# Kernel tuning notes

Hardware: AMD Instinct MI355X
Metric: run time of the kernel (lower is better)

## Reference

```python
import jax, jax.numpy as jnp
import numpy as np

DIM = 2048
K_DIM = 2048
Q_HEADS = 16
KV_HEADS = 4
HEAD_DIM = DIM // Q_HEADS  # 128
KV_DIM = HEAD_DIM * KV_HEADS  # 512
MAX_LEN = 2048
ROPE_THETA = 10000.0
ROPE_FACTOR = 8.0


def _rope_cos_sin(seq_len):
    # Faithful to generate_sin_cos_pos_emb with is_causal=True
    d = HEAD_DIM
    seq_eff = max(seq_len, MAX_LEN)
    base_adj = (ROPE_FACTOR * seq_eff / MAX_LEN - (ROPE_FACTOR - 1.0)) ** (d / (d - 2))
    adjusted_base = ROPE_THETA * base_adj
    inv_freq = 1.0 / adjusted_base ** (np.arange(0, d, 2, dtype=np.float32) / d)
    pos = np.arange(seq_len, dtype=np.float32)  # causal: no centering
    freqs = pos[:, None] * inv_freq[None, :]            # [S, d/2]
    emb = np.concatenate([freqs, freqs], axis=-1)        # [S, d]
    return jnp.asarray(np.cos(emb), jnp.float32), jnp.asarray(np.sin(emb), jnp.float32)


def _rotate_half(x):
    x1, x2 = jnp.split(x, 2, axis=-1)
    return jnp.concatenate([-x2, x1], axis=-1)


def setup_inputs() -> dict:
    key = jax.random.key(0)
    ks = jax.random.split(key, 12)
    B, S = 1, 2048
    s_in = 1.0 / np.sqrt(DIM)
    s_k = 1.0 / np.sqrt(K_DIM)
    return {
        "query": jax.random.normal(ks[0], (B, S, DIM), jnp.float32),
        "key": jax.random.normal(ks[1], (B, S, K_DIM), jnp.float32),
        "value": jax.random.normal(ks[2], (B, S, K_DIM), jnp.float32),
        "Wq": jax.random.uniform(ks[3], (DIM, DIM), jnp.float32, -s_in, s_in),
        "bq": jax.random.uniform(ks[4], (DIM,), jnp.float32, -s_in, s_in),
        "Wk": jax.random.uniform(ks[5], (KV_DIM, K_DIM), jnp.float32, -s_k, s_k),
        "bk": jax.random.uniform(ks[6], (KV_DIM,), jnp.float32, -s_k, s_k),
        "Wv": jax.random.uniform(ks[7], (KV_DIM, K_DIM), jnp.float32, -s_k, s_k),
        "bv": jax.random.uniform(ks[8], (KV_DIM,), jnp.float32, -s_k, s_k),
        "Wo": jax.random.uniform(ks[9], (DIM, DIM), jnp.float32, -s_in, s_in),
        "bo": jax.random.uniform(ks[10], (DIM,), jnp.float32, -s_in, s_in),
    }


def reference(query, key, value, Wq, bq, Wk, bk, Wv, bv, Wo, bo):
    B, S, _ = query.shape
    scale = HEAD_DIM ** -0.5

    q = query @ Wq.T + bq                                   # [B,S,DIM]
    k = key @ Wk.T + bk                                     # [B,S,KV_DIM]
    v = value @ Wv.T + bv                                   # [B,S,KV_DIM]

    q = q.reshape(B, S, Q_HEADS, HEAD_DIM)
    k = k.reshape(B, S, KV_HEADS, HEAD_DIM)
    v = v.reshape(B, S, KV_HEADS, HEAD_DIM)

    cos, sin = _rope_cos_sin(S)                              # [S,D]
    cos = cos[None, :, None, :]
    sin = sin[None, :, None, :]
    q = q * cos + _rotate_half(q) * sin
    k = k * cos + _rotate_half(k) * sin

    # [B,H,S,D]
    q = q.transpose(0, 2, 1, 3)
    k = k.transpose(0, 2, 1, 3)
    v = v.transpose(0, 2, 1, 3)

    rep = Q_HEADS // KV_HEADS
    k = jnp.repeat(k, rep, axis=1)
    v = jnp.repeat(v, rep, axis=1)

    scores = jnp.einsum('bhqd,bhkd->bhqk', q, k) * scale
    causal = jnp.tril(jnp.ones((S, S), bool))
    scores = jnp.where(causal[None, None], scores, jnp.finfo(scores.dtype).min)
    attn = jax.nn.softmax(scores, axis=-1)
    out = jnp.einsum('bhqk,bhkd->bhqd', attn, v)             # [B,H,S,D]

    out = out.transpose(0, 2, 1, 3).reshape(B, S, DIM)
    return out @ Wo.T + bo
```

## Files before the change

kernel.cpp:

```cpp
#include <hip/hip_runtime.h>
#include <stdint.h>

typedef __attribute__((ext_vector_type(8))) short short8;
typedef __attribute__((ext_vector_type(4))) float f32x4;
typedef __attribute__((ext_vector_type(4))) unsigned short u16x4;
typedef unsigned short bf16_t;

__device__ __forceinline__ bf16_t f2bf(float f) {
  union { float f; uint32_t u; } x; x.f = f;
  uint32_t r = x.u + 0x7fffu + ((x.u >> 16) & 1u);
  return (bf16_t)(r >> 16);
}

__device__ __forceinline__ void ld_g2l_16(const bf16_t* g, bf16_t* l) {
  __builtin_amdgcn_global_load_lds(
      (const __attribute__((address_space(1))) void*)g,
      (__attribute__((address_space(3))) void*)l, 16, 0, 0);
}

__global__ void rope_tab(float* __restrict__ CS, float* __restrict__ SN) {
  int idx = blockIdx.x * 256 + threadIdx.x;
  int i = idx & 63, pos = idx >> 6;
  float ang = (float)pos * exp2f((float)i * -0.2076205059f);
  CS[idx] = cosf(ang);
  SN[idx] = sinf(ang);
}

__global__ void convert_all(const float* __restrict__ s0, const float* __restrict__ s1,
                            const float* __restrict__ s2, const float* __restrict__ s3,
                            const float* __restrict__ s4, const float* __restrict__ s5,
                            const float* __restrict__ s6,
                            bf16_t* __restrict__ d0, bf16_t* __restrict__ d1,
                            bf16_t* __restrict__ d2, bf16_t* __restrict__ d3,
                            bf16_t* __restrict__ d4, bf16_t* __restrict__ d5,
                            bf16_t* __restrict__ d6) {
  int i = blockIdx.x * 256 + threadIdx.x;
  const float* src; bf16_t* dst; int off;
  if (i < 5 * 1048576) {
    int t = i >> 20; off = i & 1048575;
    if (t == 0)      { src = s0; dst = d0; }
    else if (t == 1) { src = s1; dst = d1; }
    else if (t == 2) { src = s2; dst = d2; }
    else if (t == 3) { src = s3; dst = d3; }
    else             { src = s4; dst = d4; }
  } else {
    int j = i - 5 * 1048576;
    if (j < 262144) { src = s5; dst = d5; off = j; }
    else            { src = s6; dst = d6; off = j - 262144; }
  }
  f32x4 v = *(const f32x4*)(src + (size_t)off * 4);
  u16x4 o;
  o[0] = f2bf(v[0]); o[1] = f2bf(v[1]); o[2] = f2bf(v[2]); o[3] = f2bf(v[3]);
  *(u16x4*)(dst + (size_t)off * 4) = o;
}

template <int MODE>
__device__ __forceinline__ void gemm_core(
    bf16_t* __restrict__ As, bf16_t* __restrict__ Bs,
    const bf16_t* __restrict__ A, const bf16_t* __restrict__ Bm,
    const float* __restrict__ bias, void* __restrict__ Cout,
    int N, int K, int m0, int n0,
    const float* __restrict__ CS, const float* __restrict__ SN) {
  const int tid = threadIdx.x;
  const int lane = tid & 63, quad = lane >> 4, l16 = lane & 15;
  const int wv = tid >> 6;
  const int m_off = wv * 32;
  const int c0 = tid, c1 = tid + 256;
  const int r0 = c0 >> 2, col0 = (c0 & 3) * 8;
  const int r1 = c1 >> 2, col1 = (c1 & 3) * 8;

  f32x4 acc[2][8];
  const f32x4 zf = {0.f, 0.f, 0.f, 0.f};
#pragma unroll
  for (int mi = 0; mi < 2; ++mi)
#pragma unroll
    for (int ni = 0; ni < 8; ++ni) acc[mi][ni] = zf;

  const bf16_t* Ap0 = A + (size_t)(m0 + r0) * K + col0;
  const bf16_t* Ap1 = A + (size_t)(m0 + r1) * K + col1;
  const bf16_t* Bp0 = Bm + (size_t)(n0 + r0) * K + col0;
  const bf16_t* Bp1 = Bm + (size_t)(n0 + r1) * K + col1;
  bf16_t* lA0 = As + c0 * 8;  bf16_t* lA1 = As + c1 * 8;
  bf16_t* lB0 = Bs + c0 * 8;  bf16_t* lB1 = Bs + c1 * 8;

  for (int k0 = 0; k0 < K; k0 += 32) {
    ld_g2l_16(Ap0 + k0, lA0);
    ld_g2l_16(Ap1 + k0, lA1);
    ld_g2l_16(Bp0 + k0, lB0);
    ld_g2l_16(Bp1 + k0, lB1);
    __syncthreads();
    short8 af[2], bf[8];
#pragma unroll
    for (int mi = 0; mi < 2; ++mi)
      af[mi] = *(const short8*)(&As[(m_off + mi * 16 + l16) * 32 + quad * 8]);
#pragma unroll
    for (int ni = 0; ni < 8; ++ni)
      bf[ni] = *(const short8*)(&Bs[(ni * 16 + l16) * 32 + quad * 8]);
#pragma unroll
    for (int mi = 0; mi < 2; ++mi)
#pragma unroll
      for (int ni = 0; ni < 8; ++ni)
        acc[mi][ni] = __builtin_amdgcn_mfma_f32_16x16x32_bf16(
            af[mi], bf[ni], acc[mi][ni], 0, 0, 0);
    __syncthreads();
  }

  if (MODE == 0 || MODE == 2) {
#pragma unroll
    for (int mi = 0; mi < 2; ++mi)
#pragma unroll
      for (int ni = 0; ni < 8; ++ni) {
        int n = n0 + ni * 16 + l16;
        int mbase = m0 + m_off + mi * 16 + quad * 4;
        float bv = bias[n];
#pragma unroll
        for (int r = 0; r < 4; ++r) {
          float v = acc[mi][ni][r] + bv;
          int m = mbase + r;
          if (MODE == 0) ((float*)Cout)[(size_t)m * N + n] = v;
          else           ((bf16_t*)Cout)[(size_t)n * 2048 + m] = f2bf(v);
        }
      }
  } else {
    const float scale = (MODE == 3) ? 0.08838834764831845f : 1.0f;
    bf16_t* dst = (bf16_t*)Cout;
#pragma unroll
    for (int mi = 0; mi < 2; ++mi)
#pragma unroll
      for (int r = 0; r < 4; ++r) {
        int m = m0 + m_off + mi * 16 + quad * 4 + r;
#pragma unroll
        for (int ni = 0; ni < 4; ++ni) {
          int i = ni * 16 + l16;
          int n_lo = n0 + i;
          float v1 = acc[mi][ni][r] + bias[n_lo];
          float v2 = acc[mi][ni + 4][r] + bias[n_lo + 64];
          float c = CS[m * 64 + i];
          float s = SN[m * 64 + i];
          float o1 = (v1 * c - v2 * s) * scale;
          float o2 = (v2 * c + v1 * s) * scale;
          dst[(size_t)m * N + n_lo] = f2bf(o1);
          dst[(size_t)m * N + n_lo + 64] = f2bf(o2);
        }
      }
  }
}

__global__ __launch_bounds__(256) void gemm_qkv(
    const bf16_t* __restrict__ qb, const bf16_t* __restrict__ kb,
    const bf16_t* __restrict__ vb, const bf16_t* __restrict__ wqb,
    const bf16_t* __restrict__ wkb, const bf16_t* __restrict__ wvb,
    const float* __restrict__ bq, const float* __restrict__ bk,
    const float* __restrict__ bv, bf16_t* __restrict__ Qr,
    bf16_t* __restrict__ Kr, bf16_t* __restrict__ Vt,
    const float* __restrict__ CS, const float* __restrict__ SN) {
  __shared__ __align__(16) bf16_t As[128 * 32];
  __shared__ __align__(16) bf16_t Bs[128 * 32];
  int bx = blockIdx.x, m0 = blockIdx.y * 128;
  if (bx < 16)
    gemm_core<3>(As, Bs, qb, wqb, bq, Qr, 2048, 2048, m0, bx * 128, CS, SN);
  else if (bx < 20)
    gemm_core<4>(As, Bs, kb, wkb, bk, Kr, 512, 2048, m0, (bx - 16) * 128, CS, SN);
  else
    gemm_core<2>(As, Bs, vb, wvb, bv, Vt, 512, 2048, m0, (bx - 20) * 128, CS, SN);
}

__global__ __launch_bounds__(256) void gemm_o(
    const bf16_t* __restrict__ Ob, const bf16_t* __restrict__ wob,
    const float* __restrict__ bo, float* __restrict__ out) {
  __shared__ __align__(16) bf16_t As[128 * 32];
  __shared__ __align__(16) bf16_t Bs[128 * 32];
  gemm_core<0>(As, Bs, Ob, wob, bo, out, 2048, 2048,
               blockIdx.y * 128, blockIdx.x * 128, nullptr, nullptr);
}

__global__ __launch_bounds__(256, 2) void attn_fwd(
    const bf16_t* __restrict__ Qr, const bf16_t* __restrict__ Kr,
    const bf16_t* __restrict__ Vt, bf16_t* __restrict__ Oo) {
  const int h = blockIdx.y;
  const int qt = 31 - blockIdx.x;
  const int tid = threadIdx.x;
  const int wv = tid >> 6, lane = tid & 63, quad = lane >> 4, l16 = lane & 15;
  const int q_base = qt * 64 + wv * 16;
  const int hkv = h >> 2;
  const int qg = q_base + l16;

  __shared__ __align__(16) bf16_t Ks[64 * 136];
  __shared__ __align__(16) bf16_t Vs[128 * 72];
  __shared__ __align__(16) float Sb[4][16 * 66];
  float* mys = Sb[wv];

  short8 qf[4];
  {
    const bf16_t* qp = Qr + (size_t)(q_base + l16) * 2048 + h * 128 + quad * 8;
#pragma unroll
    for (int kc = 0; kc < 4; ++kc) qf[kc] = *(const short8*)(qp + kc * 32);
  }

  const f32x4 zf = {0.f, 0.f, 0.f, 0.f};
  f32x4 o[8];
#pragma unroll
  for (int di = 0; di < 8; ++di) o[di] = zf;
  float l_acc = 0.f;

  const int ntiles = qt + 1;
  for (int t = 0; t < ntiles; ++t) {
    const int k0 = t * 64;
#pragma unroll
    for (int j = 0; j < 4; ++j) {
      int cid = tid + j * 256;
      int row = cid >> 4, c = cid & 15;
      f32x4 tmp = *(const f32x4*)(&Kr[(size_t)(k0 + row) * 512 + hkv * 128 + c * 8]);
      *(f32x4*)(&Ks[row * 136 + c * 8]) = tmp;
    }
#pragma unroll
    for (int j = 0; j < 4; ++j) {
      int cid = tid + j * 256;
      int row = cid >> 3, c = cid & 7;
      f32x4 tmp = *(const f32x4*)(&Vt[(size_t)(hkv * 128 + row) * 2048 + k0 + c * 8]);
      *(f32x4*)(&Vs[row * 72 + c * 8]) = tmp;
    }
    __syncthreads();

    f32x4 sacc[4];
#pragma unroll
    for (int sub = 0; sub < 4; ++sub) sacc[sub] = zf;
#pragma unroll
    for (int sub = 0; sub < 4; ++sub)
#pragma unroll
      for (int kc = 0; kc < 4; ++kc) {
        short8 kf = *(const short8*)(&Ks[(sub * 16 + l16) * 136 + kc * 32 + quad * 8]);
        sacc[sub] = __builtin_amdgcn_mfma_f32_16x16x32_bf16(qf[kc], kf, sacc[sub], 0, 0, 0);
      }
#pragma unroll
    for (int sub = 0; sub < 4; ++sub)
#pragma unroll
      for (int r = 0; r < 4; ++r)
        mys[(quad * 4 + r) * 66 + sub * 16 + l16] = sacc[sub][r];
    __asm__ volatile("s_waitcnt lgkmcnt(0)" ::: "memory");
    const float* rp = mys + l16 * 66 + quad * 8;
    float p0[8], p1[8];
    if (k0 + 63 > q_base) {
#pragma unroll
      for (int j = 0; j < 8; ++j) {
        int kg = k0 + quad * 8 + j;
        p0[j] = (kg <= qg) ? __expf(rp[j]) : 0.f;
        p1[j] = (kg + 32 <= qg) ? __expf(rp[32 + j]) : 0.f;
      }
    } else {
#pragma unroll
      for (int j = 0; j < 8; ++j) {
        p0[j] = __expf(rp[j]);
        p1[j] = __expf(rp[32 + j]);
      }
    }
    float ls = 0.f;
#pragma unroll
    for (int j = 0; j < 8; ++j) ls += p0[j] + p1[j];
    l_acc += ls;
    short8 pf0, pf1;
#pragma unroll
    for (int j = 0; j < 8; ++j) {
      pf0[j] = (short)f2bf(p0[j]);
      pf1[j] = (short)f2bf(p1[j]);
    }
#pragma unroll
    for (int di = 0; di < 8; ++di) {
      short8 vf0 = *(const short8*)(&Vs[(di * 16 + l16) * 72 + quad * 8]);
      short8 vf1 = *(const short8*)(&Vs[(di * 16 + l16) * 72 + 32 + quad * 8]);
      o[di] = __builtin_amdgcn_mfma_f32_16x16x32_bf16(pf0, vf0, o[di], 0, 0, 0);
      o[di] = __builtin_amdgcn_mfma_f32_16x16x32_bf16(pf1, vf1, o[di], 0, 0, 0);
    }
    __syncthreads();
  }

  float lf = l_acc;
  lf += __shfl_xor(lf, 16);
  lf += __shfl_xor(lf, 32);
  float linv[4];
#pragma unroll
  for (int r = 0; r < 4; ++r) linv[r] = 1.0f / __shfl(lf, quad * 4 + r, 64);
#pragma unroll
  for (int di = 0; di < 8; ++di)
#pragma unroll
    for (int r = 0; r < 4; ++r) {
      size_t row = q_base + quad * 4 + r;
      size_t col = h * 128 + di * 16 + l16;
      Oo[row * 2048 + col] = f2bf(o[di][r] * linv[r]);
    }
}

extern "C" void kernel_launch(void* const* d_in, const int* in_sizes, int n_in,
                              void* d_out, int out_size, void* d_ws, size_t ws_size,
                              hipStream_t stream) {
  (void)in_sizes; (void)n_in; (void)out_size; (void)ws_size;
  const float* query = (const float*)d_in[0];
  const float* key = (const float*)d_in[1];
  const float* value = (const float*)d_in[2];
  const float* Wq = (const float*)d_in[3];
  const float* bq = (const float*)d_in[4];
  const float* Wk = (const float*)d_in[5];
  const float* bk = (const float*)d_in[6];
  const float* Wv = (const float*)d_in[7];
  const float* bv = (const float*)d_in[8];
  const float* Wo = (const float*)d_in[9];
  const float* bo = (const float*)d_in[10];
  float* out = (float*)d_out;

  char* ws = (char*)d_ws;
  const size_t MB = 1024 * 1024;
  bf16_t* qb  = (bf16_t*)(ws + 0 * MB);
  bf16_t* kb  = (bf16_t*)(ws + 8 * MB);
  bf16_t* vb  = (bf16_t*)(ws + 16 * MB);
  bf16_t* wqb = (bf16_t*)(ws + 24 * MB);
  bf16_t* wkb = (bf16_t*)(ws + 32 * MB);
  bf16_t* wvb = (bf16_t*)(ws + 34 * MB);
  bf16_t* wob = (bf16_t*)(ws + 36 * MB);
  bf16_t* Qr  = (bf16_t*)(ws + 44 * MB);
  bf16_t* Kr  = (bf16_t*)(ws + 52 * MB);
  bf16_t* Vt  = (bf16_t*)(ws + 54 * MB);
  bf16_t* Ob  = (bf16_t*)(ws + 56 * MB);
  float*  CS  = (float*)(ws + 64 * MB);
  float*  SN  = (float*)(ws + 64 * MB + 512 * 1024);

  rope_tab<<<512, 256, 0, stream>>>(CS, SN);
  convert_all<<<22528, 256, 0, stream>>>(query, key, value, Wq, Wo, Wk, Wv,
                                         qb, kb, vb, wqb, wob, wkb, wvb);
  gemm_qkv<<<dim3(24, 16), 256, 0, stream>>>(qb, kb, vb, wqb, wkb, wvb,
                                             bq, bk, bv, Qr, Kr, Vt, CS, SN);
  attn_fwd<<<dim3(32, 16), 256, 0, stream>>>(Qr, Kr, Vt, Ob);
  gemm_o<<<dim3(16, 16), 256, 0, stream>>>(Ob, wob, bo, out);
}
```

Measured before the change: 303.3 us.

## Split attention KV range across two blocks and keep softmax in registers

Each causal query tile's key range is split into two halves processed by separate blocks, writing unnormalized fp32 partial outputs and row sums that a new combine kernel merges and normalizes into bf16. The score MFMA operands are swapped so probabilities stay in registers and are redistributed via ds_bpermute instead of a shared-memory round trip, removing the LDS score buffer and allowing higher occupancy. This aims to improve load balance and CU utilization at the cost of extra fp32 global traffic and an additional kernel launch.

```diff
diff --git a/kernel.cpp b/kernel.cpp
--- a/kernel.cpp
+++ b/kernel.cpp
@@ -174,11 +174,21 @@
                blockIdx.y * 128, blockIdx.x * 128, nullptr, nullptr);
 }
 
-__global__ __launch_bounds__(256, 2) void attn_fwd(
+__global__ __launch_bounds__(256, 4) void attn_fwd(
     const bf16_t* __restrict__ Qr, const bf16_t* __restrict__ Kr,
-    const bf16_t* __restrict__ Vt, bf16_t* __restrict__ Oo) {
+    const bf16_t* __restrict__ Vt, float* __restrict__ Op0,
+    float* __restrict__ Op1, float* __restrict__ Lp0,
+    float* __restrict__ Lp1) {
   const int h = blockIdx.y;
-  const int qt = 31 - blockIdx.x;
+  const int bx = blockIdx.x;
+  const int qt = 31 - (bx >> 1);
+  const int ch = bx & 1;
+  const int T = qt + 1, sp = (T + 1) >> 1;
+  const int t_beg = ch ? sp : 0;
+  const int t_end = ch ? T : sp;
+  float* __restrict__ Op = ch ? Op1 : Op0;
+  float* __restrict__ Lp = ch ? Lp1 : Lp0;
+
   const int tid = threadIdx.x;
   const int wv = tid >> 6, lane = tid & 63, quad = lane >> 4, l16 = lane & 15;
   const int q_base = qt * 64 + wv * 16;
@@ -187,12 +197,10 @@
 
   __shared__ __align__(16) bf16_t Ks[64 * 136];
   __shared__ __align__(16) bf16_t Vs[128 * 72];
-  __shared__ __align__(16) float Sb[4][16 * 66];
-  float* mys = Sb[wv];
 
   short8 qf[4];
   {
-    const bf16_t* qp = Qr + (size_t)(q_base + l16) * 2048 + h * 128 + quad * 8;
+    const bf16_t* qp = Qr + (size_t)qg * 2048 + h * 128 + quad * 8;
 #pragma unroll
     for (int kc = 0; kc < 4; ++kc) qf[kc] = *(const short8*)(qp + kc * 32);
   }
@@ -203,8 +211,7 @@
   for (int di = 0; di < 8; ++di) o[di] = zf;
   float l_acc = 0.f;
 
-  const int ntiles = qt + 1;
-  for (int t = 0; t < ntiles; ++t) {
+  for (int t = t_beg; t < t_end; ++t) {
     const int k0 = t * 64;
 #pragma unroll
     for (int j = 0; j < 4; ++j) {
@@ -230,40 +237,47 @@
 #pragma unroll
       for (int kc = 0; kc < 4; ++kc) {
         short8 kf = *(const short8*)(&Ks[(sub * 16 + l16) * 136 + kc * 32 + quad * 8]);
-        sacc[sub] = __builtin_amdgcn_mfma_f32_16x16x32_bf16(qf[kc], kf, sacc[sub], 0, 0, 0);
+        sacc[sub] = __builtin_amdgcn_mfma_f32_16x16x32_bf16(kf, qf[kc], sacc[sub], 0, 0, 0);
       }
-#pragma unroll
-    for (int sub = 0; sub < 4; ++sub)
-#pragma unroll
-      for (int r = 0; r < 4; ++r)
-        mys[(quad * 4 + r) * 66 + sub * 16 + l16] = sacc[sub][r];
-    __asm__ volatile("s_waitcnt lgkmcnt(0)" ::: "memory");
-    const float* rp = mys + l16 * 66 + quad * 8;
-    float p0[8], p1[8];
-    if (k0 + 63 > q_base) {
-#pragma unroll
-      for (int j = 0; j < 8; ++j) {
-        int kg = k0 + quad * 8 + j;
-        p0[j] = (kg <= qg) ? __expf(rp[j]) : 0.f;
-        p1[j] = (kg + 32 <= qg) ? __expf(rp[32 + j]) : 0.f;
+
+    const bool diag = (k0 + 63 > q_base);
+    uint32_t Dw[4][2];
+#pragma unroll
+    for (int sub = 0; sub < 4; ++sub) {
+      float pv[4];
+#pragma unroll
+      for (int r = 0; r < 4; ++r) {
+        float e = __expf(sacc[sub][r]);
+        if (diag) {
+          int kg = k0 + sub * 16 + quad * 4 + r;
+          if (kg > qg) e = 0.f;
+        }
+        pv[r] = e;
+        l_acc += e;
       }
-    } else {
-#pragma unroll
-      for (int j = 0; j < 8; ++j) {
-        p0[j] = __expf(rp[j]);
-        p1[j] = __expf(rp[32 + j]);
-      }
-    }
-    float ls = 0.f;
-#pragma unroll
-    for (int j = 0; j < 8; ++j) ls += p0[j] + p1[j];
-    l_acc += ls;
-    short8 pf0, pf1;
-#pragma unroll
-    for (int j = 0; j < 8; ++j) {
-      pf0[j] = (short)f2bf(p0[j]);
-      pf1[j] = (short)f2bf(p1[j]);
-    }
+      Dw[sub][0] = (uint32_t)f2bf(pv[0]) | ((uint32_t)f2bf(pv[1]) << 16);
+      Dw[sub][1] = (uint32_t)f2bf(pv[2]) | ((uint32_t)f2bf(pv[3]) << 16);
+    }
+
+    const int aA = ((((quad * 2) & 3) << 4) + l16) << 2;
+    const int aB = ((((quad * 2 + 1) & 3) << 4) + l16) << 2;
+    const bool losel = quad < 2;
+#define BPERM(a, x) ((uint32_t)__builtin_amdgcn_ds_bpermute((a), (int)(x)))
+    union { uint32_t w[4]; short8 v; } U0, U1;
+    {
+      uint32_t t0, t1;
+      t0 = BPERM(aA, Dw[0][0]); t1 = BPERM(aA, Dw[1][0]); U0.w[0] = losel ? t0 : t1;
+      t0 = BPERM(aA, Dw[0][1]); t1 = BPERM(aA, Dw[1][1]); U0.w[1] = losel ? t0 : t1;
+      t0 = BPERM(aB, Dw[0][0]); t1 = BPERM(aB, Dw[1][0]); U0.w[2] = losel ? t0 : t1;
+      t0 = BPERM(aB, Dw[0][1]); t1 = BPERM(aB, Dw[1][1]); U0.w[3] = losel ? t0 : t1;
+      t0 = BPERM(aA, Dw[2][0]); t1 = BPERM(aA, Dw[3][0]); U1.w[0] = losel ? t0 : t1;
+      t0 = BPERM(aA, Dw[2][1]); t1 = BPERM(aA, Dw[3][1]); U1.w[1] = losel ? t0 : t1;
+      t0 = BPERM(aB, Dw[2][0]); t1 = BPERM(aB, Dw[3][0]); U1.w[2] = losel ? t0 : t1;
+      t0 = BPERM(aB, Dw[2][1]); t1 = BPERM(aB, Dw[3][1]); U1.w[3] = losel ? t0 : t1;
+    }
+#undef BPERM
+    const short8 pf0 = U0.v, pf1 = U1.v;
+
 #pragma unroll
     for (int di = 0; di < 8; ++di) {
       short8 vf0 = *(const short8*)(&Vs[(di * 16 + l16) * 72 + quad * 8]);
@@ -277,17 +291,39 @@
   float lf = l_acc;
   lf += __shfl_xor(lf, 16);
   lf += __shfl_xor(lf, 32);
-  float linv[4];
-#pragma unroll
-  for (int r = 0; r < 4; ++r) linv[r] = 1.0f / __shfl(lf, quad * 4 + r, 64);
+  if (quad == 0) Lp[(h << 11) + q_base + l16] = lf;
 #pragma unroll
   for (int di = 0; di < 8; ++di)
 #pragma unroll
     for (int r = 0; r < 4; ++r) {
       size_t row = q_base + quad * 4 + r;
       size_t col = h * 128 + di * 16 + l16;
-      Oo[row * 2048 + col] = f2bf(o[di][r] * linv[r]);
-    }
+      Op[row * 2048 + col] = o[di][r];
+    }
+}
+
+__global__ __launch_bounds__(256) void attn_combine(
+    const float* __restrict__ Op0, const float* __restrict__ Op1,
+    const float* __restrict__ Lp0, const float* __restrict__ Lp1,
+    bf16_t* __restrict__ Ob) {
+  int idx = blockIdx.x * 256 + threadIdx.x;
+  size_t base = (size_t)idx * 8;
+  int row = (int)(base >> 11);
+  int col = (int)(base & 2047);
+  int h = col >> 7;
+  float li = 1.0f / (Lp0[(h << 11) + row] + Lp1[(h << 11) + row]);
+  f32x4 a0 = *(const f32x4*)(Op0 + base);
+  f32x4 a1 = *(const f32x4*)(Op0 + base + 4);
+  f32x4 b0 = *(const f32x4*)(Op1 + base);
+  f32x4 b1 = *(const f32x4*)(Op1 + base + 4);
+  u16x4 o0, o1;
+#pragma unroll
+  for (int j = 0; j < 4; ++j) {
+    o0[j] = f2bf((a0[j] + b0[j]) * li);
+    o1[j] = f2bf((a1[j] + b1[j]) * li);
+  }
+  *(u16x4*)(Ob + base) = o0;
+  *(u16x4*)(Ob + base + 4) = o1;
 }
 
 extern "C" void kernel_launch(void* const* d_in, const int* in_sizes, int n_in,
@@ -323,11 +359,17 @@
   float*  CS  = (float*)(ws + 64 * MB);
   float*  SN  = (float*)(ws + 64 * MB + 512 * 1024);
 
+  float* Op0 = (float*)(ws + 0 * MB);
+  float* Op1 = (float*)(ws + 16 * MB);
+  float* Lp0 = (float*)(ws + 32 * MB);
+  float* Lp1 = (float*)(ws + 32 * MB + 256 * 1024);
+
   rope_tab<<<512, 256, 0, stream>>>(CS, SN);
   convert_all<<<22528, 256, 0, stream>>>(query, key, value, Wq, Wo, Wk, Wv,
                                          qb, kb, vb, wqb, wob, wkb, wvb);
   gemm_qkv<<<dim3(24, 16), 256, 0, stream>>>(qb, kb, vb, wqb, wkb, wvb,
                                              bq, bk, bv, Qr, Kr, Vt, CS, SN);
-  attn_fwd<<<dim3(32, 16), 256, 0, stream>>>(Qr, Kr, Vt, Ob);
+  attn_fwd<<<dim3(64, 16), 256, 0, stream>>>(Qr, Kr, Vt, Op0, Op1, Lp0, Lp1);
+  attn_combine<<<2048, 256, 0, stream>>>(Op0, Op1, Lp0, Lp1, Ob);
   gemm_o<<<dim3(16, 16), 256, 0, stream>>>(Ob, wob, bo, out);
 }
```

New measurement: 318.3 us. 4.9% more time.
